# Optimization experiments

Hardware: AMD Instinct MI355X
Metric: run time of the kernel (lower is better)

The kernel has to match this reference:

```python
import jax, jax.numpy as jnp
import numpy as np

BS, N_PTS, N_SAMPLES = 8, 8192, 2048
GRID_SIZE = 4096
MAX_X, MAX_Y, MAX_Z = 25.0, 25.0, 5.0
P_NORM = 1


def _sample_axis(key, max_v):
    # linspace(-max_v, max_v, GRID_SIZE) indexed by multinomial(uniform, replacement=False)
    rng = jnp.linspace(-max_v, max_v, GRID_SIZE, dtype=jnp.float32)
    idx = jax.random.choice(key, GRID_SIZE, (N_SAMPLES,), replace=False)
    return rng[idx]


def setup_inputs() -> dict:
    key = jax.random.key(0)
    k1, k2, kx, ky, kz = jax.random.split(key, 5)
    gts = jax.random.normal(k1, (BS, N_PTS, 3), dtype=jnp.float32) * 10.0
    preds = jax.random.normal(k2, (BS, N_PTS, 3), dtype=jnp.float32) * 10.0
    gx = _sample_axis(kx, MAX_X)
    gy = _sample_axis(ky, MAX_Y)
    gz = _sample_axis(kz, MAX_Z)
    grid = jnp.stack([gx, gy, gz], axis=1)  # (N_SAMPLES, 3)
    grid_points = jnp.broadcast_to(grid[None], (BS, N_SAMPLES, 3)).astype(jnp.float32)
    return {"gts": gts, "preds": preds, "grid_points": grid_points}


def _cdist(x, y):
    # Euclidean cdist: (b, n, d) x (b, m, d) -> (b, n, m)
    x2 = jnp.sum(x * x, axis=-1)[:, :, None]
    y2 = jnp.sum(y * y, axis=-1)[:, None, :]
    xy = jnp.einsum('bnd,bmd->bnm', x, y)
    return jnp.sqrt(jnp.maximum(x2 + y2 - 2.0 * xy, 0.0))


def reference(gts, preds, grid_points):
    mins = jnp.min(_cdist(grid_points, preds), axis=2)   # (b, n_samples)
    mins2 = jnp.min(_cdist(grid_points, gts), axis=2)    # (b, n_samples)
    diff = jnp.abs(mins - mins2)
    if P_NORM == 2:
        diff = diff ** 2
    return jnp.mean(diff, axis=1)  # (b,)
```

## Files before the change

### kernel.cpp

```cpp
#include <hip/hip_runtime.h>
#include <math.h>

#define BS 8
#define N_PTS 8192
#define N_SAMPLES 2048
#define TA 512
#define SPT 4
#define PSPLIT 64
#define CHUNK (N_PTS / PSPLIT)

#define PART_ELEMS (2 * BS * PSPLIT * N_SAMPLES)

__global__ __launch_bounds__(TA, 4)
void chamfer_min_kernel(const float* __restrict__ gts,
                        const float* __restrict__ preds,
                        const float* __restrict__ grid,
                        float* __restrict__ part)
{
    const int bid = blockIdx.x;
    const int b   = bid >> 6;
    const int pc  = bid & (PSPLIT - 1);
    const int t   = threadIdx.x;

    __shared__ float4 ldsP[CHUNK];
    __shared__ float4 ldsG[CHUNK];

    if (t < 2 * CHUNK) {
        const int j = t & (CHUNK - 1);
        const float* src = ((t < CHUNK) ? preds : gts)
                         + ((size_t)b * N_PTS + (size_t)pc * CHUNK + j) * 3;
        const float x = src[0], y = src[1], z = src[2];
        const float4 v = make_float4(x, y, z, fmaf(x, x, fmaf(y, y, z * z)));
        if (t < CHUNK) ldsP[j] = v; else ldsG[j] = v;
    }

    float nsx[SPT], nsy[SPT], nsz[SPT], mP[SPT], mG[SPT];
    {
        const float* grow = grid + (size_t)b * N_SAMPLES * 3;
#pragma unroll
        for (int k = 0; k < SPT; ++k) {
            const int s = k * TA + t;
            nsx[k] = -2.0f * grow[s * 3 + 0];
            nsy[k] = -2.0f * grow[s * 3 + 1];
            nsz[k] = -2.0f * grow[s * 3 + 2];
            mP[k] = 3.0e38f;
            mG[k] = 3.0e38f;
        }
    }

    __syncthreads();

#pragma unroll 4
    for (int j = 0; j < CHUNK; j += 2) {
        const float4 p0 = ldsP[j], p1 = ldsP[j + 1];
        const float4 g0 = ldsG[j], g1 = ldsG[j + 1];
#pragma unroll
        for (int k = 0; k < SPT; ++k) {
            const float x = nsx[k], y = nsy[k], z = nsz[k];
            const float t0 = fmaf(p0.x, x, fmaf(p0.y, y, fmaf(p0.z, z, p0.w)));
            const float t1 = fmaf(p1.x, x, fmaf(p1.y, y, fmaf(p1.z, z, p1.w)));
            mP[k] = fminf(fminf(t0, t1), mP[k]);
            const float u0 = fmaf(g0.x, x, fmaf(g0.y, y, fmaf(g0.z, z, g0.w)));
            const float u1 = fmaf(g1.x, x, fmaf(g1.y, y, fmaf(g1.z, z, g1.w)));
            mG[k] = fminf(fminf(u0, u1), mG[k]);
        }
    }

    float* pp = part + (((size_t)b)        * PSPLIT + pc) * N_SAMPLES;
    float* pg = part + (((size_t)(BS + b)) * PSPLIT + pc) * N_SAMPLES;
#pragma unroll
    for (int k = 0; k < SPT; ++k) {
        const int s = k * TA + t;
        const float s2 = 0.25f * fmaf(nsx[k], nsx[k], fmaf(nsy[k], nsy[k], nsz[k] * nsz[k]));
        pp[s] = fmaxf(mP[k] + s2, 0.0f);
        pg[s] = fmaxf(mG[k] + s2, 0.0f);
    }
}

__global__ __launch_bounds__(256, 1)
void chamfer_reduce_kernel(const float* __restrict__ part,
                           float* __restrict__ tsum)
{
    const int blk  = blockIdx.x;
    const int b    = blk >> 3;
    const int tile = blk & 7;
    const int t    = threadIdx.x;
    const int s    = tile * 256 + t;

    const float* pp = part + ((size_t)b)        * PSPLIT * N_SAMPLES + s;
    const float* pg = part + ((size_t)(BS + b)) * PSPLIT * N_SAMPLES + s;

    float mp = 3.0e38f, mg = 3.0e38f;
#pragma unroll 8
    for (int pc = 0; pc < PSPLIT; ++pc) {
        mp = fminf(mp, pp[(size_t)pc * N_SAMPLES]);
        mg = fminf(mg, pg[(size_t)pc * N_SAMPLES]);
    }

    float v = fabsf(sqrtf(mp) - sqrtf(mg));

#pragma unroll
    for (int off = 32; off > 0; off >>= 1)
        v += __shfl_down(v, off, 64);

    __shared__ float w[4];
    if ((t & 63) == 0) w[t >> 6] = v;
    __syncthreads();
    if (t == 0) tsum[blk] = (w[0] + w[1]) + (w[2] + w[3]);
}

__global__ __launch_bounds__(64)
void chamfer_out_kernel(const float* __restrict__ tsum,
                        float* __restrict__ out)
{
    const int b = threadIdx.x;
    if (b < BS) {
        float tot = 0.0f;
#pragma unroll
        for (int i = 0; i < 8; ++i) tot += tsum[b * 8 + i];
        out[b] = tot * (1.0f / (float)N_SAMPLES);
    }
}

extern "C" void kernel_launch(void* const* d_in, const int* in_sizes, int n_in,
                              void* d_out, int out_size, void* d_ws, size_t ws_size,
                              hipStream_t stream)
{
    const float* gts   = (const float*)d_in[0];
    const float* preds = (const float*)d_in[1];
    const float* grid  = (const float*)d_in[2];
    float* out  = (float*)d_out;
    float* part = (float*)d_ws;
    float* tsum = part + PART_ELEMS;

    chamfer_min_kernel<<<dim3(BS * PSPLIT), dim3(TA), 0, stream>>>(gts, preds, grid, part);
    chamfer_reduce_kernel<<<dim3(64), dim3(256), 0, stream>>>(part, tsum);
    chamfer_out_kernel<<<dim3(1), dim3(64), 0, stream>>>(tsum, out);
}
```

Baseline: 36.17 us.

## Use packed FMA and min3 in the distance loop, and vectorize the reduce kernel

Reorganizes the shared-memory point layout into x/y/z/w pairs so each distance evaluation can use packed two-wide FMAs (v_pk_fma_f32). The three-way minimum becomes a single v_min3 instruction, aiming to roughly halve the VALU instruction count of the hot loop. The reduce kernel now reads float4 vectors with 16 blocks instead of 64, which cuts the number of load instructions but leaves fewer blocks, and so less parallelism, for that stage. The output kernel is updated to match the new partial-sum layout.

```diff
diff --git a/kernel.cpp b/kernel.cpp
--- a/kernel.cpp
+++ b/kernel.cpp
@@ -8,8 +8,27 @@
 #define SPT 4
 #define PSPLIT 64
 #define CHUNK (N_PTS / PSPLIT)
+#define NPAIR (CHUNK / 2)
 
 #define PART_ELEMS (2 * BS * PSPLIT * N_SAMPLES)
+
+typedef float v2f __attribute__((ext_vector_type(2)));
+
+#if !defined(__has_builtin) || !__has_builtin(__builtin_elementwise_fma)
+static __device__ inline v2f pk_fma(v2f a, v2f b, v2f c) {
+    v2f r; r.x = fmaf(a.x, b.x, c.x); r.y = fmaf(a.y, b.y, c.y); return r;
+}
+#else
+#define pk_fma(a, b, c) __builtin_elementwise_fma((a), (b), (c))
+#endif
+
+static __device__ inline float min3(float a, float b, float c) {
+    float r;
+    asm("v_min3_f32 %0, %1, %2, %3" : "=v"(r) : "v"(a), "v"(b), "v"(c));
+    return r;
+}
+
+struct __align__(16) PairT { v2f xx, yy, zz, ww; };
 
 __global__ __launch_bounds__(TA, 4)
 void chamfer_min_kernel(const float* __restrict__ gts,
@@ -22,16 +41,22 @@
     const int pc  = bid & (PSPLIT - 1);
     const int t   = threadIdx.x;
 
-    __shared__ float4 ldsP[CHUNK];
-    __shared__ float4 ldsG[CHUNK];
+    __shared__ PairT ldsP[NPAIR];
+    __shared__ PairT ldsG[NPAIR];
 
-    if (t < 2 * CHUNK) {
-        const int j = t & (CHUNK - 1);
-        const float* src = ((t < CHUNK) ? preds : gts)
-                         + ((size_t)b * N_PTS + (size_t)pc * CHUNK + j) * 3;
-        const float x = src[0], y = src[1], z = src[2];
-        const float4 v = make_float4(x, y, z, fmaf(x, x, fmaf(y, y, z * z)));
-        if (t < CHUNK) ldsP[j] = v; else ldsG[j] = v;
+    if (t < 2 * NPAIR) {
+        const int j = t & (NPAIR - 1);
+        const float* src = ((t < NPAIR) ? preds : gts)
+                         + ((size_t)b * N_PTS + (size_t)pc * CHUNK + 2 * j) * 3;
+        const float x0 = src[0], y0 = src[1], z0 = src[2];
+        const float x1 = src[3], y1 = src[4], z1 = src[5];
+        PairT pr;
+        pr.xx = (v2f){x0, x1};
+        pr.yy = (v2f){y0, y1};
+        pr.zz = (v2f){z0, z1};
+        pr.ww = (v2f){fmaf(x0, x0, fmaf(y0, y0, z0 * z0)),
+                      fmaf(x1, x1, fmaf(y1, y1, z1 * z1))};
+        if (t < NPAIR) ldsP[j] = pr; else ldsG[j] = pr;
     }
 
     float nsx[SPT], nsy[SPT], nsz[SPT], mP[SPT], mG[SPT];
@@ -51,18 +76,18 @@
     __syncthreads();
 
 #pragma unroll 4
-    for (int j = 0; j < CHUNK; j += 2) {
-        const float4 p0 = ldsP[j], p1 = ldsP[j + 1];
-        const float4 g0 = ldsG[j], g1 = ldsG[j + 1];
+    for (int j = 0; j < NPAIR; ++j) {
+        const PairT p = ldsP[j];
+        const PairT g = ldsG[j];
 #pragma unroll
         for (int k = 0; k < SPT; ++k) {
-            const float x = nsx[k], y = nsy[k], z = nsz[k];
-            const float t0 = fmaf(p0.x, x, fmaf(p0.y, y, fmaf(p0.z, z, p0.w)));
-            const float t1 = fmaf(p1.x, x, fmaf(p1.y, y, fmaf(p1.z, z, p1.w)));
-            mP[k] = fminf(fminf(t0, t1), mP[k]);
-            const float u0 = fmaf(g0.x, x, fmaf(g0.y, y, fmaf(g0.z, z, g0.w)));
-            const float u1 = fmaf(g1.x, x, fmaf(g1.y, y, fmaf(g1.z, z, g1.w)));
-            mG[k] = fminf(fminf(u0, u1), mG[k]);
+            const v2f vx = {nsx[k], nsx[k]};
+            const v2f vy = {nsy[k], nsy[k]};
+            const v2f vz = {nsz[k], nsz[k]};
+            const v2f tp = pk_fma(p.xx, vx, pk_fma(p.yy, vy, pk_fma(p.zz, vz, p.ww)));
+            mP[k] = min3(tp.x, tp.y, mP[k]);
+            const v2f tg = pk_fma(g.xx, vx, pk_fma(g.yy, vy, pk_fma(g.zz, vz, g.ww)));
+            mG[k] = min3(tg.x, tg.y, mG[k]);
         }
     }
 
@@ -82,22 +107,30 @@
                            float* __restrict__ tsum)
 {
     const int blk  = blockIdx.x;
-    const int b    = blk >> 3;
-    const int tile = blk & 7;
+    const int b    = blk >> 1;
+    const int half = blk & 1;
     const int t    = threadIdx.x;
-    const int s    = tile * 256 + t;
+    const int g    = half * 256 + t;
 
-    const float* pp = part + ((size_t)b)        * PSPLIT * N_SAMPLES + s;
-    const float* pg = part + ((size_t)(BS + b)) * PSPLIT * N_SAMPLES + s;
+    const float4* pp = (const float4*)(part + ((size_t)b)        * PSPLIT * N_SAMPLES) + g;
+    const float4* pg = (const float4*)(part + ((size_t)(BS + b)) * PSPLIT * N_SAMPLES) + g;
 
-    float mp = 3.0e38f, mg = 3.0e38f;
+    float4 mp = make_float4(3.0e38f, 3.0e38f, 3.0e38f, 3.0e38f);
+    float4 mg = mp;
 #pragma unroll 8
     for (int pc = 0; pc < PSPLIT; ++pc) {
-        mp = fminf(mp, pp[(size_t)pc * N_SAMPLES]);
-        mg = fminf(mg, pg[(size_t)pc * N_SAMPLES]);
+        const float4 a = pp[(size_t)pc * (N_SAMPLES / 4)];
+        mp.x = fminf(mp.x, a.x); mp.y = fminf(mp.y, a.y);
+        mp.z = fminf(mp.z, a.z); mp.w = fminf(mp.w, a.w);
+        const float4 c = pg[(size_t)pc * (N_SAMPLES / 4)];
+        mg.x = fminf(mg.x, c.x); mg.y = fminf(mg.y, c.y);
+        mg.z = fminf(mg.z, c.z); mg.w = fminf(mg.w, c.w);
     }
 
-    float v = fabsf(sqrtf(mp) - sqrtf(mg));
+    float v = fabsf(sqrtf(mp.x) - sqrtf(mg.x))
+            + fabsf(sqrtf(mp.y) - sqrtf(mg.y))
+            + fabsf(sqrtf(mp.z) - sqrtf(mg.z))
+            + fabsf(sqrtf(mp.w) - sqrtf(mg.w));
 
 #pragma unroll
     for (int off = 32; off > 0; off >>= 1)
@@ -114,12 +147,8 @@
                         float* __restrict__ out)
 {
     const int b = threadIdx.x;
-    if (b < BS) {
-        float tot = 0.0f;
-#pragma unroll
-        for (int i = 0; i < 8; ++i) tot += tsum[b * 8 + i];
-        out[b] = tot * (1.0f / (float)N_SAMPLES);
-    }
+    if (b < BS)
+        out[b] = (tsum[2 * b] + tsum[2 * b + 1]) * (1.0f / (float)N_SAMPLES);
 }
 
 extern "C" void kernel_launch(void* const* d_in, const int* in_sizes, int n_in,
@@ -134,6 +163,6 @@
     float* tsum = part + PART_ELEMS;
 
     chamfer_min_kernel<<<dim3(BS * PSPLIT), dim3(TA), 0, stream>>>(gts, preds, grid, part);
-    chamfer_reduce_kernel<<<dim3(64), dim3(256), 0, stream>>>(part, tsum);
+    chamfer_reduce_kernel<<<dim3(16), dim3(256), 0, stream>>>(part, tsum);
     chamfer_out_kernel<<<dim3(1), dim3(64), 0, stream>>>(tsum, out);
 }
```

After: 38.94 us. 7.6% more time.

## Double point split, shrink blocks, and use two-stage hierarchical min reduction

Applied to the files above, without the earlier changes.

The min kernel now uses 128 point chunks of 64 points with 256 threads, each thread handling 8 samples, which gives 1024 blocks and more register reuse per LDS load. The single reduction is replaced by two stages: a wide float4 reduction over groups of 8 partials into 16 segments across 128 blocks, then a small kernel that finishes the min and computes the per-batch abs difference. The point is to spread the larger partial-result reduction over more of the GPU. In exchange it doubles the partial buffer traffic and adds one more kernel launch.

```diff
diff --git a/kernel.cpp b/kernel.cpp
--- a/kernel.cpp
+++ b/kernel.cpp
@@ -4,12 +4,14 @@
 #define BS 8
 #define N_PTS 8192
 #define N_SAMPLES 2048
-#define TA 512
-#define SPT 4
-#define PSPLIT 64
+#define TA 256
+#define SPT 8
+#define PSPLIT 128
 #define CHUNK (N_PTS / PSPLIT)
+#define NSEG 16
 
 #define PART_ELEMS (2 * BS * PSPLIT * N_SAMPLES)
+#define MID_ELEMS  (2 * BS * NSEG * N_SAMPLES)
 
 __global__ __launch_bounds__(TA, 4)
 void chamfer_min_kernel(const float* __restrict__ gts,
@@ -18,7 +20,7 @@
                         float* __restrict__ part)
 {
     const int bid = blockIdx.x;
-    const int b   = bid >> 6;
+    const int b   = bid >> 7;
     const int pc  = bid & (PSPLIT - 1);
     const int t   = threadIdx.x;
 
@@ -78,26 +80,63 @@
 }
 
 __global__ __launch_bounds__(256, 1)
-void chamfer_reduce_kernel(const float* __restrict__ part,
-                           float* __restrict__ tsum)
+void chamfer_red1_kernel(const float* __restrict__ part,
+                         float* __restrict__ mid)
+{
+    const int blk = blockIdx.x;
+    const int b   = blk >> 4;
+    const int seg = blk & (NSEG - 1);
+    const int t   = threadIdx.x;
+    const int pc0 = seg * (PSPLIT / NSEG);
+
+    const float4* pp = (const float4*)(part + ((size_t)b        * PSPLIT + pc0) * N_SAMPLES);
+    const float4* pg = (const float4*)(part + ((size_t)(BS + b) * PSPLIT + pc0) * N_SAMPLES);
+    float4* mp4 = (float4*)(mid + ((size_t)b        * NSEG + seg) * N_SAMPLES);
+    float4* mg4 = (float4*)(mid + ((size_t)(BS + b) * NSEG + seg) * N_SAMPLES);
+
+#pragma unroll
+    for (int c = 0; c < 2; ++c) {
+        const int g = c * 256 + t;
+        float4 mp = make_float4(3.0e38f, 3.0e38f, 3.0e38f, 3.0e38f);
+        float4 mg = mp;
+#pragma unroll
+        for (int r = 0; r < PSPLIT / NSEG; ++r) {
+            const float4 a = pp[(size_t)r * (N_SAMPLES / 4) + g];
+            mp.x = fminf(mp.x, a.x); mp.y = fminf(mp.y, a.y);
+            mp.z = fminf(mp.z, a.z); mp.w = fminf(mp.w, a.w);
+            const float4 d = pg[(size_t)r * (N_SAMPLES / 4) + g];
+            mg.x = fminf(mg.x, d.x); mg.y = fminf(mg.y, d.y);
+            mg.z = fminf(mg.z, d.z); mg.w = fminf(mg.w, d.w);
+        }
+        mp4[g] = mp;
+        mg4[g] = mg;
+    }
+}
+
+__global__ __launch_bounds__(256, 1)
+void chamfer_red2_kernel(const float* __restrict__ mid,
+                         float* __restrict__ tsum)
 {
     const int blk  = blockIdx.x;
-    const int b    = blk >> 3;
-    const int tile = blk & 7;
+    const int b    = blk >> 1;
+    const int half = blk & 1;
     const int t    = threadIdx.x;
-    const int s    = tile * 256 + t;
 
-    const float* pp = part + ((size_t)b)        * PSPLIT * N_SAMPLES + s;
-    const float* pg = part + ((size_t)(BS + b)) * PSPLIT * N_SAMPLES + s;
+    const float* mp = mid + ((size_t)b        * NSEG) * N_SAMPLES;
+    const float* mg = mid + ((size_t)(BS + b) * NSEG) * N_SAMPLES;
 
-    float mp = 3.0e38f, mg = 3.0e38f;
-#pragma unroll 8
-    for (int pc = 0; pc < PSPLIT; ++pc) {
-        mp = fminf(mp, pp[(size_t)pc * N_SAMPLES]);
-        mg = fminf(mg, pg[(size_t)pc * N_SAMPLES]);
+    float v = 0.0f;
+#pragma unroll
+    for (int k = 0; k < 4; ++k) {
+        const int s = half * 1024 + k * 256 + t;
+        float a = 3.0e38f, c = 3.0e38f;
+#pragma unroll
+        for (int seg = 0; seg < NSEG; ++seg) {
+            a = fminf(a, mp[(size_t)seg * N_SAMPLES + s]);
+            c = fminf(c, mg[(size_t)seg * N_SAMPLES + s]);
+        }
+        v += fabsf(sqrtf(a) - sqrtf(c));
     }
-
-    float v = fabsf(sqrtf(mp) - sqrtf(mg));
 
 #pragma unroll
     for (int off = 32; off > 0; off >>= 1)
@@ -114,12 +153,8 @@
                         float* __restrict__ out)
 {
     const int b = threadIdx.x;
-    if (b < BS) {
-        float tot = 0.0f;
-#pragma unroll
-        for (int i = 0; i < 8; ++i) tot += tsum[b * 8 + i];
-        out[b] = tot * (1.0f / (float)N_SAMPLES);
-    }
+    if (b < BS)
+        out[b] = (tsum[2 * b] + tsum[2 * b + 1]) * (1.0f / (float)N_SAMPLES);
 }
 
 extern "C" void kernel_launch(void* const* d_in, const int* in_sizes, int n_in,
@@ -131,9 +166,11 @@
     const float* grid  = (const float*)d_in[2];
     float* out  = (float*)d_out;
     float* part = (float*)d_ws;
-    float* tsum = part + PART_ELEMS;
+    float* mid  = part + PART_ELEMS;
+    float* tsum = mid + MID_ELEMS;
 
     chamfer_min_kernel<<<dim3(BS * PSPLIT), dim3(TA), 0, stream>>>(gts, preds, grid, part);
-    chamfer_reduce_kernel<<<dim3(64), dim3(256), 0, stream>>>(part, tsum);
+    chamfer_red1_kernel<<<dim3(BS * NSEG), dim3(256), 0, stream>>>(part, mid);
+    chamfer_red2_kernel<<<dim3(16), dim3(256), 0, stream>>>(mid, tsum);
     chamfer_out_kernel<<<dim3(1), dim3(64), 0, stream>>>(tsum, out);
 }
```

Measured after the change: 53.16 us. +46.9%, slower.
